# Optimization experiments

Measured on AMD Instinct MI355X. Metric: run time of the kernel, lower is better.

Reference implementation:

```python
import jax, jax.numpy as jnp
import numpy as np

TEMPERATURE = 0.1
NEG_INF = -1e30  # finite sentinel to keep logsumexp grad-safe


def setup_inputs() -> dict:
    key = jax.random.key(0)
    k_emb, k_lab = jax.random.split(key)
    B, D, C = 8192, 256, 100
    embeddings = jax.random.normal(k_emb, (B, D), dtype=jnp.float32)
    labels = jax.random.randint(k_lab, (B,), 0, C, dtype=jnp.int64)
    return {"embeddings": embeddings, "labels": labels}


def reference(embeddings, labels):
    B = embeddings.shape[0]
    # squared L2 pairwise distance: ||x_i||^2 + ||x_j||^2 - 2 x_i . x_j
    sq = jnp.sum(embeddings * embeddings, axis=1)  # [B]
    gram = jnp.einsum('id,jd->ij', embeddings, embeddings)  # [B,B]
    dist2 = jnp.maximum(sq[:, None] + sq[None, :] - 2.0 * gram, 0.0)
    sim = -dist2 / TEMPERATURE  # [B,B]

    same = labels[:, None] == labels[None, :]
    eye = jnp.eye(B, dtype=bool)
    pos_mask = same & ~eye
    neg_mask = ~same

    # per-row uniform random positive via Gumbel-argmax over pos_mask
    k_sel = jax.random.key(42)
    g = jax.random.gumbel(k_sel, (B, B), dtype=jnp.float32)
    j = jnp.argmax(jnp.where(pos_mask, g, -jnp.inf), axis=1)  # [B]

    numerator = jnp.take_along_axis(sim, j[:, None], axis=1)[:, 0]  # sim[i, j_i]
    denominator = jax.nn.logsumexp(jnp.where(neg_mask, sim, NEG_INF), axis=1)

    valid = pos_mask.any(axis=1) & neg_mask.any(axis=1)
    per_row = -(numerator - denominator)
    n_valid = jnp.sum(valid)
    loss = jnp.sum(jnp.where(valid, per_row, 0.0)) / jnp.maximum(n_valid, 1)
    return jnp.where(n_valid > 0, loss, 0.0)
```

## Files before the change

### kernel.cpp

```cpp
#include <hip/hip_runtime.h>
#include <float.h>
#include <math.h>


#define B_N 8192
#define D_K 256
#define NCLS 100
#define MAXC 512
#define NSPLIT 16
#define NPART NSPLIT
#define JR (B_N / NSPLIT)
#define BI 128
#define BJ 128
#define NJT (JR / BJ)
#define BK 64
#define NKC (D_K / BK)
#define NEG_INF -1e30f

typedef __attribute__((ext_vector_type(8))) short bf16x8;
typedef __attribute__((ext_vector_type(4))) float f32x4;
typedef unsigned short ushort_t;

__device__ __forceinline__ unsigned rotl32(unsigned x, int d){ return (x << d) | (x >> (32 - d)); }

__device__ __forceinline__ float gumbel_at(unsigned idx){
  const unsigned HALF = (unsigned)B_N * (unsigned)B_N / 2u;
  unsigned c0, c1; bool second;
  if (idx < HALF){ c0 = idx; c1 = idx + HALF; second = false; }
  else            { c0 = idx - HALF; c1 = idx; second = true; }
  const unsigned ks0 = 0u, ks1 = 42u, ks2 = 0u ^ 42u ^ 0x1BD11BDAu;
  unsigned x0 = c0 + ks0, x1 = c1 + ks1;
#define TF_RND(r) { x0 += x1; x1 = rotl32(x1, (r)); x1 ^= x0; }
  TF_RND(13) TF_RND(15) TF_RND(26) TF_RND(6)   x0 += ks1; x1 += ks2 + 1u;
  TF_RND(17) TF_RND(29) TF_RND(16) TF_RND(24)  x0 += ks2; x1 += ks0 + 2u;
  TF_RND(13) TF_RND(15) TF_RND(26) TF_RND(6)   x0 += ks0; x1 += ks1 + 3u;
  TF_RND(17) TF_RND(29) TF_RND(16) TF_RND(24)  x0 += ks1; x1 += ks2 + 4u;
  TF_RND(13) TF_RND(15) TF_RND(26) TF_RND(6)   x0 += ks2; x1 += ks0 + 5u;
#undef TF_RND
  unsigned bits = second ? x1 : x0;
  float u = __uint_as_float((bits >> 9) | 0x3f800000u) - 1.0f;
  const float TINY = 1.17549435e-38f;
  u = u * (1.0f - TINY) + TINY;
  u = fmaxf(TINY, u);
  return -logf(-logf(u));
}

__device__ __forceinline__ ushort_t f2bf(float x){
  unsigned u = __float_as_uint(x);
  return (ushort_t)((u + 0x7FFFu + ((u >> 16) & 1u)) >> 16);
}

__device__ __forceinline__ void async16(const ushort_t* g, ushort_t* lds_wave_base){
  __builtin_amdgcn_global_load_lds((const __attribute__((address_space(1))) void*)g,
                                   (__attribute__((address_space(3))) void*)lds_wave_base,
                                   16, 0, 0);
}

__global__ void prep_kernel(const float* __restrict__ E, ushort_t* __restrict__ Ebf,
                            float* __restrict__ sq, float* __restrict__ acc4){
  if (blockIdx.x == 0 && threadIdx.x < 4)
    acc4[threadIdx.x] = 0.f;
  int w = threadIdx.x >> 6, lane = threadIdx.x & 63;
  int row = blockIdx.x * 4 + w;
  const float4 v = *reinterpret_cast<const float4*>(E + (size_t)row * D_K + lane * 4);
  float s = v.x*v.x + v.y*v.y + v.z*v.z + v.w*v.w;
#pragma unroll
  for (int off = 32; off > 0; off >>= 1) s += __shfl_down(s, off);
  if (lane == 0) sq[row] = s;
  ushort4 o; o.x = f2bf(v.x); o.y = f2bf(v.y); o.z = f2bf(v.z); o.w = f2bf(v.w);
  *reinterpret_cast<ushort4*>(Ebf + (size_t)row * D_K + lane * 4) = o;
}

__global__ __launch_bounds__(256)
void classsel_kernel(const int* __restrict__ labels, int* __restrict__ jsel){
  __shared__ int s_list[MAXC];
  __shared__ int s_n;
  const int c = blockIdx.x;
  const int tid = threadIdx.x;
  if (tid == 0) s_n = 0;
  __syncthreads();
  for (int t = tid; t < B_N; t += 256){
    if (labels[t] == c){
      int p = atomicAdd(&s_n, 1);
      if (p < MAXC) s_list[p] = t;
    }
  }
  __syncthreads();
  const int n = min(s_n, MAXC);
  for (int rowIdx = tid; rowIdx < n; rowIdx += 256){
    const int row = s_list[rowIdx];
    float gb = -FLT_MAX; int jb = -1;
    for (int t = 0; t < n; t++){
      int j = s_list[t];
      if (j != row){
        float g = gumbel_at(((unsigned)row << 13) + (unsigned)j);
        if (g > gb || (g == gb && (unsigned)j < (unsigned)jb)){ gb = g; jb = j; }
      }
    }
    jsel[row] = jb;
  }
}

__global__ __launch_bounds__(256, 2)
void fused_kernel(const ushort_t* __restrict__ Ebf, const int* __restrict__ labels,
                  const float* __restrict__ sq, const int* __restrict__ jsel,
                  float* __restrict__ numer,
                  float* __restrict__ wsM, float* __restrict__ wsS)
{
  __shared__ __align__(16) ushort_t Bs[NKC][BJ * BK];
  __shared__ float s_sqj[JR];
  __shared__ int   s_lj[JR];
  __shared__ float s_sqi[BI];
  __shared__ int   s_li[BI];
  __shared__ int   s_ji[BI];

  const int bi    = blockIdx.x >> 4;
  const int split = blockIdx.x & 15;
  const int i0    = bi * BI;
  const int jbase = split * JR;
  const int tid   = threadIdx.x;
  const int lane  = tid & 63;
  const int w     = tid >> 6;
  const int quad  = lane >> 4;
  const int l15   = lane & 15;

  for (int t = tid; t < JR; t += 256){ s_sqj[t] = sq[jbase + t]; s_lj[t] = labels[jbase + t]; }
  if (tid < BI){ s_sqi[tid] = sq[i0 + tid]; s_li[tid] = labels[i0 + tid]; s_ji[tid] = jsel[i0 + tid]; }

  bf16x8 af[2][8];
#pragma unroll
  for (int mt = 0; mt < 2; mt++){
    const ushort_t* rp = Ebf + (size_t)(i0 + w * 32 + mt * 16 + l15) * D_K + quad * 8;
#pragma unroll
    for (int c = 0; c < 8; c++)
      af[mt][c] = *reinterpret_cast<const bf16x8*>(rp + c * 32);
  }

  float sm[8], ssum[8];
#pragma unroll
  for (int r = 0; r < 8; r++){ sm[r] = NEG_INF; ssum[r] = 0.f; }

  __syncthreads();

  for (int jt = 0; jt < NJT; jt++){
    const int j0 = jbase + jt * BJ;
    f32x4 acc[2][8];
#pragma unroll
    for (int mt = 0; mt < 2; mt++)
#pragma unroll
      for (int nt = 0; nt < 8; nt++) acc[mt][nt] = (f32x4)0.f;

    __syncthreads();
#pragma unroll
    for (int kc = 0; kc < NKC; kc++){
#pragma unroll
      for (int rd = 0; rd < 4; rd++){
        int slot = rd * 256 + tid;
        int r = slot >> 3, gs = slot & 7;
        int gsrc = (gs ^ (r & 7)) << 3;
        ushort_t* ldsB = &Bs[kc][(size_t)(rd * 256 + w * 64) * 8];
        async16(Ebf + (size_t)(j0 + r) * D_K + kc * BK + gsrc, ldsB);
      }
    }
    __syncthreads();

#pragma unroll
    for (int kc = 0; kc < NKC; kc++){
#pragma unroll
      for (int s = 0; s < 2; s++){
        const int g = s * 4 + quad;
        const int c = kc * 2 + s;
        bf16x8 bfr[8];
#pragma unroll
        for (int nt = 0; nt < 8; nt++){
          int r = nt * 16 + l15;
          bfr[nt] = *reinterpret_cast<const bf16x8*>(&Bs[kc][r * BK + ((g ^ (r & 7)) << 3)]);
        }
#pragma unroll
        for (int nt = 0; nt < 8; nt++){
          acc[0][nt] = __builtin_amdgcn_mfma_f32_16x16x32_bf16(af[0][c], bfr[nt], acc[0][nt], 0, 0, 0);
          acc[1][nt] = __builtin_amdgcn_mfma_f32_16x16x32_bf16(af[1][c], bfr[nt], acc[1][nt], 0, 0, 0);
        }
      }
    }

    float sqj[8]; int lj[8];
#pragma unroll
    for (int nt = 0; nt < 8; nt++){
      int ccol = jt * BJ + nt * 16 + l15;
      sqj[nt] = s_sqj[ccol]; lj[nt] = s_lj[ccol];
    }
#pragma unroll
    for (int mt = 0; mt < 2; mt++){
#pragma unroll
      for (int rr = 0; rr < 4; rr++){
        int rl = w * 32 + mt * 16 + quad * 4 + rr;
        float sqv = s_sqi[rl]; int lrow = s_li[rl]; int jsl = s_ji[rl];
        int sidx = mt * 4 + rr;
        float sv[8];
#pragma unroll
        for (int nt = 0; nt < 8; nt++){
          float a = acc[mt][nt][rr];
          float simv = -10.f * fmaxf(fmaf(-2.f, a, sqv + sqj[nt]), 0.f);
          int colg = j0 + nt * 16 + l15;
          if (colg == jsl) numer[i0 + rl] = simv;
          sv[nt] = (lj[nt] != lrow) ? simv : NEG_INF;
        }
        float m8 = fmaxf(fmaxf(fmaxf(sv[0],sv[1]),fmaxf(sv[2],sv[3])),
                         fmaxf(fmaxf(sv[4],sv[5]),fmaxf(sv[6],sv[7])));
        float s8 = __expf(sv[0]-m8)+__expf(sv[1]-m8)+__expf(sv[2]-m8)+__expf(sv[3]-m8)
                 + __expf(sv[4]-m8)+__expf(sv[5]-m8)+__expf(sv[6]-m8)+__expf(sv[7]-m8);
        float M = fmaxf(sm[sidx], m8);
        ssum[sidx] = ssum[sidx]*__expf(sm[sidx]-M) + s8*__expf(m8-M);
        sm[sidx] = M;
      }
    }
  }

#pragma unroll
  for (int sidx = 0; sidx < 8; sidx++){
    float mv = sm[sidx], sv2 = ssum[sidx];
#pragma unroll
    for (int mask = 1; mask < 16; mask <<= 1){
      float m2 = __shfl_xor(mv, mask);
      float s2 = __shfl_xor(sv2, mask);
      float M = fmaxf(mv, m2);
      sv2 = sv2 * __expf(mv - M) + s2 * __expf(m2 - M);
      mv = M;
    }
    if (l15 == 0){
      int mt = sidx >> 2, rr = sidx & 3;
      int rl = w * 32 + mt * 16 + quad * 4 + rr;
      int o = split * B_N + i0 + rl;
      wsM[o] = mv; wsS[o] = sv2;
    }
  }
}

__global__ __launch_bounds__(256)
void finale_kernel(const float* __restrict__ wsM, const float* __restrict__ wsS,
                   const float* __restrict__ numer, const int* __restrict__ jsel,
                   float* __restrict__ acc4, float* __restrict__ out)
{
  const int tid = threadIdx.x;
  const int row = blockIdx.x * 256 + tid;
  float M = -3.0e38f, S = 0.f;
#pragma unroll
  for (int p = 0; p < NPART; p++){
    float m2 = wsM[p * B_N + row], s2 = wsS[p * B_N + row];
    float Mn = fmaxf(M, m2);
    S = S * __expf(M - Mn) + s2 * __expf(m2 - Mn);
    M = Mn;
  }
  bool v = (jsel[row] >= 0) && (M > -5e29f);
  float s = v ? (M + logf(S) - numer[row]) : 0.f;
  unsigned n = v ? 1u : 0u;
#pragma unroll
  for (int off = 32; off > 0; off >>= 1){ s += __shfl_down(s, off); n += __shfl_down(n, off); }
  __shared__ float ssm[4]; __shared__ unsigned snm[4];
  if ((tid & 63) == 0){ ssm[tid >> 6] = s; snm[tid >> 6] = n; }
  __syncthreads();
  if (tid == 0){
    float bs = ssm[0] + ssm[1] + ssm[2] + ssm[3];
    unsigned bn = snm[0] + snm[1] + snm[2] + snm[3];
    atomicAdd(&acc4[0], bs);
    atomicAdd((unsigned*)&acc4[1], bn);
    __threadfence();
    unsigned old = atomicAdd((unsigned*)&acc4[2], 1u);
    if (old == 31u){
      float St = atomicAdd(&acc4[0], 0.f);
      unsigned Nt = atomicAdd((unsigned*)&acc4[1], 0u);
      out[0] = (Nt > 0u) ? (St / (float)Nt) : 0.f;
    }
  }
}

extern "C" void kernel_launch(void* const* d_in, const int* in_sizes, int n_in,
                              void* d_out, int out_size, void* d_ws, size_t ws_size,
                              hipStream_t stream)
{
  const float* E      = (const float*)d_in[0];
  const int*   labels = (const int*)d_in[1];
  float*       out    = (float*)d_out;

  ushort_t* Ebf = (ushort_t*)d_ws;
  float* wsM    = (float*)(Ebf + (size_t)B_N * D_K);
  float* wsS    = wsM + NPART * B_N;
  float* sqb    = wsS + NPART * B_N;
  float* numer  = sqb + B_N;
  int* jsel     = (int*)(numer + B_N);
  float* acc4   = (float*)(jsel + B_N);

  prep_kernel<<<B_N / 4, 256, 0, stream>>>(E, Ebf, sqb, acc4);
  classsel_kernel<<<NCLS, 256, 0, stream>>>(labels, jsel);
  fused_kernel<<<(B_N / BI) * NSPLIT, 256, 0, stream>>>(Ebf, labels, sqb, jsel, numer, wsM, wsS);
  finale_kernel<<<B_N / 256, 256, 0, stream>>>(wsM, wsS, numer, jsel, acc4, out);
}
```

Measured before the change: 164.2 us.

## Use 2x2 wave tiling, single-stage LDS buffer, fewer splits, merge prep kernels

The fused kernel now arranges its four waves in a 2x2 grid over the 128x128 tile, so each wave holds 64 rows of A fragments and reads only 64 columns of B from LDS. This halves B-fragment LDS reads per MFMA. The LDS B buffer drops from four K-chunks to one, with a sync before and after each chunk load, which adds barriers and removes the overlap between loads and MFMAs. NSPLIT falls from 16 to 8, giving fewer, longer blocks (512 instead of 1024), and each wave column writes its own partial logsumexp slot. The prep and class-selection kernels are merged into one launch to save launch overhead.

```diff
diff --git a/kernel.cpp b/kernel.cpp
--- a/kernel.cpp
+++ b/kernel.cpp
@@ -7,8 +7,8 @@
 #define D_K 256
 #define NCLS 100
 #define MAXC 512
-#define NSPLIT 16
-#define NPART NSPLIT
+#define NSPLIT 8
+#define NPART (NSPLIT * 2)
 #define JR (B_N / NSPLIT)
 #define BI 128
 #define BJ 128
@@ -16,6 +16,7 @@
 #define BK 64
 #define NKC (D_K / BK)
 #define NEG_INF -1e30f
+#define PREP_BLOCKS (B_N / 4)
 
 typedef __attribute__((ext_vector_type(8))) short bf16x8;
 typedef __attribute__((ext_vector_type(4))) float f32x4;
@@ -56,27 +57,27 @@
                                    16, 0, 0);
 }
 
-__global__ void prep_kernel(const float* __restrict__ E, ushort_t* __restrict__ Ebf,
-                            float* __restrict__ sq, float* __restrict__ acc4){
-  if (blockIdx.x == 0 && threadIdx.x < 4)
-    acc4[threadIdx.x] = 0.f;
-  int w = threadIdx.x >> 6, lane = threadIdx.x & 63;
-  int row = blockIdx.x * 4 + w;
-  const float4 v = *reinterpret_cast<const float4*>(E + (size_t)row * D_K + lane * 4);
-  float s = v.x*v.x + v.y*v.y + v.z*v.z + v.w*v.w;
-#pragma unroll
-  for (int off = 32; off > 0; off >>= 1) s += __shfl_down(s, off);
-  if (lane == 0) sq[row] = s;
-  ushort4 o; o.x = f2bf(v.x); o.y = f2bf(v.y); o.z = f2bf(v.z); o.w = f2bf(v.w);
-  *reinterpret_cast<ushort4*>(Ebf + (size_t)row * D_K + lane * 4) = o;
-}
-
 __global__ __launch_bounds__(256)
-void classsel_kernel(const int* __restrict__ labels, int* __restrict__ jsel){
+void prepsel_kernel(const float* __restrict__ E, const int* __restrict__ labels,
+                    ushort_t* __restrict__ Ebf, float* __restrict__ sq,
+                    int* __restrict__ jsel, float* __restrict__ acc4){
+  const int tid = threadIdx.x;
+  if (blockIdx.x < PREP_BLOCKS){
+    if (blockIdx.x == 0 && tid < 4) acc4[tid] = 0.f;
+    int w = tid >> 6, lane = tid & 63;
+    int row = blockIdx.x * 4 + w;
+    const float4 v = *reinterpret_cast<const float4*>(E + (size_t)row * D_K + lane * 4);
+    float s = v.x*v.x + v.y*v.y + v.z*v.z + v.w*v.w;
+#pragma unroll
+    for (int off = 32; off > 0; off >>= 1) s += __shfl_down(s, off);
+    if (lane == 0) sq[row] = s;
+    ushort4 o; o.x = f2bf(v.x); o.y = f2bf(v.y); o.z = f2bf(v.z); o.w = f2bf(v.w);
+    *reinterpret_cast<ushort4*>(Ebf + (size_t)row * D_K + lane * 4) = o;
+    return;
+  }
   __shared__ int s_list[MAXC];
   __shared__ int s_n;
-  const int c = blockIdx.x;
-  const int tid = threadIdx.x;
+  const int c = blockIdx.x - PREP_BLOCKS;
   if (tid == 0) s_n = 0;
   __syncthreads();
   for (int t = tid; t < B_N; t += 256){
@@ -107,118 +108,114 @@
                   float* __restrict__ numer,
                   float* __restrict__ wsM, float* __restrict__ wsS)
 {
-  __shared__ __align__(16) ushort_t Bs[NKC][BJ * BK];
+  __shared__ __align__(16) ushort_t Bs[BJ * BK];
   __shared__ float s_sqj[JR];
   __shared__ int   s_lj[JR];
   __shared__ float s_sqi[BI];
   __shared__ int   s_li[BI];
   __shared__ int   s_ji[BI];
 
-  const int bi    = blockIdx.x >> 4;
-  const int split = blockIdx.x & 15;
+  const int bi    = blockIdx.x >> 3;
+  const int split = blockIdx.x & 7;
   const int i0    = bi * BI;
   const int jbase = split * JR;
   const int tid   = threadIdx.x;
   const int lane  = tid & 63;
   const int w     = tid >> 6;
+  const int wy    = w >> 1;
+  const int wx    = w & 1;
   const int quad  = lane >> 4;
   const int l15   = lane & 15;
 
   for (int t = tid; t < JR; t += 256){ s_sqj[t] = sq[jbase + t]; s_lj[t] = labels[jbase + t]; }
   if (tid < BI){ s_sqi[tid] = sq[i0 + tid]; s_li[tid] = labels[i0 + tid]; s_ji[tid] = jsel[i0 + tid]; }
 
-  bf16x8 af[2][8];
-#pragma unroll
-  for (int mt = 0; mt < 2; mt++){
-    const ushort_t* rp = Ebf + (size_t)(i0 + w * 32 + mt * 16 + l15) * D_K + quad * 8;
+  bf16x8 af[4][8];
+#pragma unroll
+  for (int mt = 0; mt < 4; mt++){
+    const ushort_t* rp = Ebf + (size_t)(i0 + wy * 64 + mt * 16 + l15) * D_K + quad * 8;
 #pragma unroll
     for (int c = 0; c < 8; c++)
       af[mt][c] = *reinterpret_cast<const bf16x8*>(rp + c * 32);
   }
 
-  float sm[8], ssum[8];
-#pragma unroll
-  for (int r = 0; r < 8; r++){ sm[r] = NEG_INF; ssum[r] = 0.f; }
+  float sm[16], ssum[16];
+#pragma unroll
+  for (int r = 0; r < 16; r++){ sm[r] = NEG_INF; ssum[r] = 0.f; }
 
   __syncthreads();
 
   for (int jt = 0; jt < NJT; jt++){
     const int j0 = jbase + jt * BJ;
-    f32x4 acc[2][8];
-#pragma unroll
-    for (int mt = 0; mt < 2; mt++)
-#pragma unroll
-      for (int nt = 0; nt < 8; nt++) acc[mt][nt] = (f32x4)0.f;
-
-    __syncthreads();
-#pragma unroll
+    f32x4 acc[4][4];
+#pragma unroll
+    for (int mt = 0; mt < 4; mt++)
+#pragma unroll
+      for (int nt = 0; nt < 4; nt++) acc[mt][nt] = (f32x4)0.f;
+
     for (int kc = 0; kc < NKC; kc++){
+      const int koff = kc * BK;
+      __syncthreads();
 #pragma unroll
       for (int rd = 0; rd < 4; rd++){
         int slot = rd * 256 + tid;
         int r = slot >> 3, gs = slot & 7;
         int gsrc = (gs ^ (r & 7)) << 3;
-        ushort_t* ldsB = &Bs[kc][(size_t)(rd * 256 + w * 64) * 8];
-        async16(Ebf + (size_t)(j0 + r) * D_K + kc * BK + gsrc, ldsB);
-      }
-    }
-    __syncthreads();
-
-#pragma unroll
-    for (int kc = 0; kc < NKC; kc++){
+        ushort_t* ldsB = Bs + (size_t)(rd * 256 + w * 64) * 8;
+        async16(Ebf + (size_t)(j0 + r) * D_K + koff + gsrc, ldsB);
+      }
+      __syncthreads();
 #pragma unroll
       for (int s = 0; s < 2; s++){
         const int g = s * 4 + quad;
         const int c = kc * 2 + s;
-        bf16x8 bfr[8];
-#pragma unroll
-        for (int nt = 0; nt < 8; nt++){
-          int r = nt * 16 + l15;
-          bfr[nt] = *reinterpret_cast<const bf16x8*>(&Bs[kc][r * BK + ((g ^ (r & 7)) << 3)]);
+        bf16x8 bfr[4];
+#pragma unroll
+        for (int nt = 0; nt < 4; nt++){
+          int r = wx * 64 + nt * 16 + l15;
+          bfr[nt] = *reinterpret_cast<const bf16x8*>(&Bs[r * BK + ((g ^ (r & 7)) << 3)]);
         }
 #pragma unroll
-        for (int nt = 0; nt < 8; nt++){
-          acc[0][nt] = __builtin_amdgcn_mfma_f32_16x16x32_bf16(af[0][c], bfr[nt], acc[0][nt], 0, 0, 0);
-          acc[1][nt] = __builtin_amdgcn_mfma_f32_16x16x32_bf16(af[1][c], bfr[nt], acc[1][nt], 0, 0, 0);
-        }
-      }
-    }
-
-    float sqj[8]; int lj[8];
-#pragma unroll
-    for (int nt = 0; nt < 8; nt++){
-      int ccol = jt * BJ + nt * 16 + l15;
+        for (int mt = 0; mt < 4; mt++)
+#pragma unroll
+          for (int nt = 0; nt < 4; nt++)
+            acc[mt][nt] = __builtin_amdgcn_mfma_f32_16x16x32_bf16(af[mt][c], bfr[nt], acc[mt][nt], 0, 0, 0);
+      }
+    }
+
+    float sqj[4]; int lj[4];
+#pragma unroll
+    for (int nt = 0; nt < 4; nt++){
+      int ccol = jt * BJ + wx * 64 + nt * 16 + l15;
       sqj[nt] = s_sqj[ccol]; lj[nt] = s_lj[ccol];
     }
 #pragma unroll
-    for (int mt = 0; mt < 2; mt++){
+    for (int mt = 0; mt < 4; mt++){
 #pragma unroll
       for (int rr = 0; rr < 4; rr++){
-        int rl = w * 32 + mt * 16 + quad * 4 + rr;
+        int rl = wy * 64 + mt * 16 + quad * 4 + rr;
         float sqv = s_sqi[rl]; int lrow = s_li[rl]; int jsl = s_ji[rl];
         int sidx = mt * 4 + rr;
-        float sv[8];
-#pragma unroll
-        for (int nt = 0; nt < 8; nt++){
+        float sv[4];
+#pragma unroll
+        for (int nt = 0; nt < 4; nt++){
           float a = acc[mt][nt][rr];
           float simv = -10.f * fmaxf(fmaf(-2.f, a, sqv + sqj[nt]), 0.f);
-          int colg = j0 + nt * 16 + l15;
+          int colg = j0 + wx * 64 + nt * 16 + l15;
           if (colg == jsl) numer[i0 + rl] = simv;
           sv[nt] = (lj[nt] != lrow) ? simv : NEG_INF;
         }
-        float m8 = fmaxf(fmaxf(fmaxf(sv[0],sv[1]),fmaxf(sv[2],sv[3])),
-                         fmaxf(fmaxf(sv[4],sv[5]),fmaxf(sv[6],sv[7])));
-        float s8 = __expf(sv[0]-m8)+__expf(sv[1]-m8)+__expf(sv[2]-m8)+__expf(sv[3]-m8)
-                 + __expf(sv[4]-m8)+__expf(sv[5]-m8)+__expf(sv[6]-m8)+__expf(sv[7]-m8);
-        float M = fmaxf(sm[sidx], m8);
-        ssum[sidx] = ssum[sidx]*__expf(sm[sidx]-M) + s8*__expf(m8-M);
+        float m4 = fmaxf(fmaxf(sv[0], sv[1]), fmaxf(sv[2], sv[3]));
+        float s4 = __expf(sv[0]-m4) + __expf(sv[1]-m4) + __expf(sv[2]-m4) + __expf(sv[3]-m4);
+        float M = fmaxf(sm[sidx], m4);
+        ssum[sidx] = ssum[sidx]*__expf(sm[sidx]-M) + s4*__expf(m4-M);
         sm[sidx] = M;
       }
     }
   }
 
 #pragma unroll
-  for (int sidx = 0; sidx < 8; sidx++){
+  for (int sidx = 0; sidx < 16; sidx++){
     float mv = sm[sidx], sv2 = ssum[sidx];
 #pragma unroll
     for (int mask = 1; mask < 16; mask <<= 1){
@@ -230,8 +227,8 @@
     }
     if (l15 == 0){
       int mt = sidx >> 2, rr = sidx & 3;
-      int rl = w * 32 + mt * 16 + quad * 4 + rr;
-      int o = split * B_N + i0 + rl;
+      int rl = wy * 64 + mt * 16 + quad * 4 + rr;
+      int o = (split * 2 + wx) * B_N + i0 + rl;
       wsM[o] = mv; wsS[o] = sv2;
     }
   }
@@ -291,8 +288,7 @@
   int* jsel     = (int*)(numer + B_N);
   float* acc4   = (float*)(jsel + B_N);
 
-  prep_kernel<<<B_N / 4, 256, 0, stream>>>(E, Ebf, sqb, acc4);
-  classsel_kernel<<<NCLS, 256, 0, stream>>>(labels, jsel);
+  prepsel_kernel<<<PREP_BLOCKS + NCLS, 256, 0, stream>>>(E, labels, Ebf, sqb, jsel, acc4);
   fused_kernel<<<(B_N / BI) * NSPLIT, 256, 0, stream>>>(Ebf, labels, sqb, jsel, numer, wsM, wsS);
   finale_kernel<<<B_N / 256, 256, 0, stream>>>(wsM, wsS, numer, jsel, acc4, out);
 }
```

Result: slower. 196.0 us (+19.4%).

## Double-buffer B tiles, merge prep/select kernels, fold finale into fused kernel

Applied to the files above, without the earlier changes.

Replaces the load-all-then-compute B staging with a two-slot ring buffer, so the async load of the next k-chunk overlaps MFMA work on the current one. Halves the j-split count, which gives fewer, longer blocks and fewer partial rows to merge. Merges the prep and class-select kernels into one launch and moves the final reduction into the last-finishing fused block via an atomic ticket, removing two launches. The risks are a serial single-block finale over all 8192 rows and a smaller grid (512 blocks) that may underfill the GPU.

```diff
diff --git a/kernel.cpp b/kernel.cpp
--- a/kernel.cpp
+++ b/kernel.cpp
@@ -7,7 +7,7 @@
 #define D_K 256
 #define NCLS 100
 #define MAXC 512
-#define NSPLIT 16
+#define NSPLIT 8
 #define NPART NSPLIT
 #define JR (B_N / NSPLIT)
 #define BI 128
@@ -15,7 +15,10 @@
 #define NJT (JR / BJ)
 #define BK 64
 #define NKC (D_K / BK)
+#define NSTEP (NJT * NKC)
 #define NEG_INF -1e30f
+#define PREP_BLOCKS (B_N / 4)
+#define GRID_FUSED ((B_N / BI) * NSPLIT)
 
 typedef __attribute__((ext_vector_type(8))) short bf16x8;
 typedef __attribute__((ext_vector_type(4))) float f32x4;
@@ -56,27 +59,39 @@
                                    16, 0, 0);
 }
 
-__global__ void prep_kernel(const float* __restrict__ E, ushort_t* __restrict__ Ebf,
-                            float* __restrict__ sq, float* __restrict__ acc4){
-  if (blockIdx.x == 0 && threadIdx.x < 4)
-    acc4[threadIdx.x] = 0.f;
-  int w = threadIdx.x >> 6, lane = threadIdx.x & 63;
-  int row = blockIdx.x * 4 + w;
-  const float4 v = *reinterpret_cast<const float4*>(E + (size_t)row * D_K + lane * 4);
-  float s = v.x*v.x + v.y*v.y + v.z*v.z + v.w*v.w;
-#pragma unroll
-  for (int off = 32; off > 0; off >>= 1) s += __shfl_down(s, off);
-  if (lane == 0) sq[row] = s;
-  ushort4 o; o.x = f2bf(v.x); o.y = f2bf(v.y); o.z = f2bf(v.z); o.w = f2bf(v.w);
-  *reinterpret_cast<ushort4*>(Ebf + (size_t)row * D_K + lane * 4) = o;
+__device__ __forceinline__ void stageB(const ushort_t* __restrict__ Ebf, int j0, int koff,
+                                       ushort_t* buf, int tid, int w){
+#pragma unroll
+  for (int rd = 0; rd < 4; rd++){
+    int slot = rd * 256 + tid;
+    int r = slot >> 3, gs = slot & 7;
+    int gsrc = (gs ^ (r & 7)) << 3;
+    ushort_t* ldsB = buf + (size_t)(rd * 256 + w * 64) * 8;
+    async16(Ebf + (size_t)(j0 + r) * D_K + koff + gsrc, ldsB);
+  }
 }
 
 __global__ __launch_bounds__(256)
-void classsel_kernel(const int* __restrict__ labels, int* __restrict__ jsel){
+void prepsel_kernel(const float* __restrict__ E, const int* __restrict__ labels,
+                    ushort_t* __restrict__ Ebf, float* __restrict__ sq,
+                    int* __restrict__ jsel, float* __restrict__ acc4){
+  const int tid = threadIdx.x;
+  if (blockIdx.x < PREP_BLOCKS){
+    if (blockIdx.x == 0 && tid < 4) acc4[tid] = 0.f;
+    int w = tid >> 6, lane = tid & 63;
+    int row = blockIdx.x * 4 + w;
+    const float4 v = *reinterpret_cast<const float4*>(E + (size_t)row * D_K + lane * 4);
+    float s = v.x*v.x + v.y*v.y + v.z*v.z + v.w*v.w;
+#pragma unroll
+    for (int off = 32; off > 0; off >>= 1) s += __shfl_down(s, off);
+    if (lane == 0) sq[row] = s;
+    ushort4 o; o.x = f2bf(v.x); o.y = f2bf(v.y); o.z = f2bf(v.z); o.w = f2bf(v.w);
+    *reinterpret_cast<ushort4*>(Ebf + (size_t)row * D_K + lane * 4) = o;
+    return;
+  }
   __shared__ int s_list[MAXC];
   __shared__ int s_n;
-  const int c = blockIdx.x;
-  const int tid = threadIdx.x;
+  const int c = blockIdx.x - PREP_BLOCKS;
   if (tid == 0) s_n = 0;
   __syncthreads();
   for (int t = tid; t < B_N; t += 256){
@@ -105,17 +120,20 @@
 void fused_kernel(const ushort_t* __restrict__ Ebf, const int* __restrict__ labels,
                   const float* __restrict__ sq, const int* __restrict__ jsel,
                   float* __restrict__ numer,
-                  float* __restrict__ wsM, float* __restrict__ wsS)
+                  float* __restrict__ wsM, float* __restrict__ wsS,
+                  float* __restrict__ acc4, float* __restrict__ out)
 {
-  __shared__ __align__(16) ushort_t Bs[NKC][BJ * BK];
+  __shared__ __align__(16) ushort_t Bs[2][BJ * BK];
   __shared__ float s_sqj[JR];
   __shared__ int   s_lj[JR];
   __shared__ float s_sqi[BI];
   __shared__ int   s_li[BI];
   __shared__ int   s_ji[BI];
-
-  const int bi    = blockIdx.x >> 4;
-  const int split = blockIdx.x & 15;
+  __shared__ unsigned s_tk;
+  __shared__ float ssm[4]; __shared__ unsigned snm[4];
+
+  const int bi    = blockIdx.x >> 3;
+  const int split = blockIdx.x & 7;
   const int i0    = bi * BI;
   const int jbase = split * JR;
   const int tid   = threadIdx.x;
@@ -140,7 +158,7 @@
 #pragma unroll
   for (int r = 0; r < 8; r++){ sm[r] = NEG_INF; ssum[r] = 0.f; }
 
-  __syncthreads();
+  stageB(Ebf, jbase, 0, Bs[0], tid, w);
 
   for (int jt = 0; jt < NJT; jt++){
     const int j0 = jbase + jt * BJ;
@@ -150,36 +168,30 @@
 #pragma unroll
       for (int nt = 0; nt < 8; nt++) acc[mt][nt] = (f32x4)0.f;
 
-    __syncthreads();
 #pragma unroll
     for (int kc = 0; kc < NKC; kc++){
-#pragma unroll
-      for (int rd = 0; rd < 4; rd++){
-        int slot = rd * 256 + tid;
-        int r = slot >> 3, gs = slot & 7;
-        int gsrc = (gs ^ (r & 7)) << 3;
-        ushort_t* ldsB = &Bs[kc][(size_t)(rd * 256 + w * 64) * 8];
-        async16(Ebf + (size_t)(j0 + r) * D_K + kc * BK + gsrc, ldsB);
-      }
-    }
-    __syncthreads();
-
-#pragma unroll
-    for (int kc = 0; kc < NKC; kc++){
+      const int cur = kc & 1;
+      __syncthreads();
+      {
+        int step = jt * NKC + kc + 1;
+        if (step < NSTEP){
+          int njt = step >> 2, nkc = step & 3;
+          stageB(Ebf, jbase + njt * BJ, nkc * BK, Bs[cur ^ 1], tid, w);
+        }
+      }
 #pragma unroll
       for (int s = 0; s < 2; s++){
         const int g = s * 4 + quad;
-        const int c = kc * 2 + s;
         bf16x8 bfr[8];
 #pragma unroll
         for (int nt = 0; nt < 8; nt++){
           int r = nt * 16 + l15;
-          bfr[nt] = *reinterpret_cast<const bf16x8*>(&Bs[kc][r * BK + ((g ^ (r & 7)) << 3)]);
+          bfr[nt] = *reinterpret_cast<const bf16x8*>(&Bs[cur][r * BK + ((g ^ (r & 7)) << 3)]);
         }
 #pragma unroll
         for (int nt = 0; nt < 8; nt++){
-          acc[0][nt] = __builtin_amdgcn_mfma_f32_16x16x32_bf16(af[0][c], bfr[nt], acc[0][nt], 0, 0, 0);
-          acc[1][nt] = __builtin_amdgcn_mfma_f32_16x16x32_bf16(af[1][c], bfr[nt], acc[1][nt], 0, 0, 0);
+          acc[0][nt] = __builtin_amdgcn_mfma_f32_16x16x32_bf16(af[0][kc * 2 + s], bfr[nt], acc[0][nt], 0, 0, 0);
+          acc[1][nt] = __builtin_amdgcn_mfma_f32_16x16x32_bf16(af[1][kc * 2 + s], bfr[nt], acc[1][nt], 0, 0, 0);
         }
       }
     }
@@ -235,41 +247,32 @@
       wsM[o] = mv; wsS[o] = sv2;
     }
   }
-}
-
-__global__ __launch_bounds__(256)
-void finale_kernel(const float* __restrict__ wsM, const float* __restrict__ wsS,
-                   const float* __restrict__ numer, const int* __restrict__ jsel,
-                   float* __restrict__ acc4, float* __restrict__ out)
-{
-  const int tid = threadIdx.x;
-  const int row = blockIdx.x * 256 + tid;
-  float M = -3.0e38f, S = 0.f;
-#pragma unroll
-  for (int p = 0; p < NPART; p++){
-    float m2 = wsM[p * B_N + row], s2 = wsS[p * B_N + row];
-    float Mn = fmaxf(M, m2);
-    S = S * __expf(M - Mn) + s2 * __expf(m2 - Mn);
-    M = Mn;
-  }
-  bool v = (jsel[row] >= 0) && (M > -5e29f);
-  float s = v ? (M + logf(S) - numer[row]) : 0.f;
-  unsigned n = v ? 1u : 0u;
-#pragma unroll
-  for (int off = 32; off > 0; off >>= 1){ s += __shfl_down(s, off); n += __shfl_down(n, off); }
-  __shared__ float ssm[4]; __shared__ unsigned snm[4];
-  if ((tid & 63) == 0){ ssm[tid >> 6] = s; snm[tid >> 6] = n; }
+
+  __threadfence();
+  if (tid == 0) s_tk = atomicAdd((unsigned*)acc4 + 3, 1u);
   __syncthreads();
-  if (tid == 0){
-    float bs = ssm[0] + ssm[1] + ssm[2] + ssm[3];
-    unsigned bn = snm[0] + snm[1] + snm[2] + snm[3];
-    atomicAdd(&acc4[0], bs);
-    atomicAdd((unsigned*)&acc4[1], bn);
+  if (s_tk == (unsigned)(GRID_FUSED - 1)){
     __threadfence();
-    unsigned old = atomicAdd((unsigned*)&acc4[2], 1u);
-    if (old == 31u){
-      float St = atomicAdd(&acc4[0], 0.f);
-      unsigned Nt = atomicAdd((unsigned*)&acc4[1], 0u);
+    float s = 0.f; unsigned n = 0u;
+    for (int row = tid; row < B_N; row += 256){
+      float M = -3.0e38f, S = 0.f;
+#pragma unroll
+      for (int p = 0; p < NPART; p++){
+        float m2 = wsM[p * B_N + row], s2 = wsS[p * B_N + row];
+        float Mn = fmaxf(M, m2);
+        S = S * __expf(M - Mn) + s2 * __expf(m2 - Mn);
+        M = Mn;
+      }
+      bool v = (jsel[row] >= 0) && (M > -5e29f);
+      if (v){ s += M + logf(S) - numer[row]; n += 1u; }
+    }
+#pragma unroll
+    for (int off = 32; off > 0; off >>= 1){ s += __shfl_down(s, off); n += __shfl_down(n, off); }
+    if ((tid & 63) == 0){ ssm[tid >> 6] = s; snm[tid >> 6] = n; }
+    __syncthreads();
+    if (tid == 0){
+      float St = ssm[0] + ssm[1] + ssm[2] + ssm[3];
+      unsigned Nt = snm[0] + snm[1] + snm[2] + snm[3];
       out[0] = (Nt > 0u) ? (St / (float)Nt) : 0.f;
     }
   }
@@ -291,8 +294,6 @@
   int* jsel     = (int*)(numer + B_N);
   float* acc4   = (float*)(jsel + B_N);
 
-  prep_kernel<<<B_N / 4, 256, 0, stream>>>(E, Ebf, sqb, acc4);
-  classsel_kernel<<<NCLS, 256, 0, stream>>>(labels, jsel);
-  fused_kernel<<<(B_N / BI) * NSPLIT, 256, 0, stream>>>(Ebf, labels, sqb, jsel, numer, wsM, wsS);
-  finale_kernel<<<B_N / 256, 256, 0, stream>>>(wsM, wsS, numer, jsel, acc4, out);
-}
+  prepsel_kernel<<<PREP_BLOCKS + NCLS, 256, 0, stream>>>(E, labels, Ebf, sqb, jsel, acc4);
+  fused_kernel<<<GRID_FUSED, 256, 0, stream>>>(Ebf, labels, sqb, jsel, numer, wsM, wsS, acc4, out);
+}
```

Result: slower. 236.3 us (+43.9%).

## Merge prep and class-select kernels; shrink B tile LDS to one K-chunk

Applied to the files above, without the earlier changes.

Folds the bf16 conversion/norm kernel and the per-class Gumbel selection kernel into one launch, so the two independent jobs share a grid and one kernel launch is dropped. In the fused GEMM kernel, the B tile LDS buffer shrinks from all four K-chunks to a single chunk, reloaded per chunk with barriers around it. This cuts LDS use, which may allow more resident blocks, but adds synchronisation and serialises load and compute within each j-tile.

```diff
diff --git a/kernel.cpp b/kernel.cpp
--- a/kernel.cpp
+++ b/kernel.cpp
@@ -16,6 +16,7 @@
 #define BK 64
 #define NKC (D_K / BK)
 #define NEG_INF -1e30f
+#define PREP_BLOCKS (B_N / 4)
 
 typedef __attribute__((ext_vector_type(8))) short bf16x8;
 typedef __attribute__((ext_vector_type(4))) float f32x4;
@@ -56,27 +57,27 @@
                                    16, 0, 0);
 }
 
-__global__ void prep_kernel(const float* __restrict__ E, ushort_t* __restrict__ Ebf,
-                            float* __restrict__ sq, float* __restrict__ acc4){
-  if (blockIdx.x == 0 && threadIdx.x < 4)
-    acc4[threadIdx.x] = 0.f;
-  int w = threadIdx.x >> 6, lane = threadIdx.x & 63;
-  int row = blockIdx.x * 4 + w;
-  const float4 v = *reinterpret_cast<const float4*>(E + (size_t)row * D_K + lane * 4);
-  float s = v.x*v.x + v.y*v.y + v.z*v.z + v.w*v.w;
-#pragma unroll
-  for (int off = 32; off > 0; off >>= 1) s += __shfl_down(s, off);
-  if (lane == 0) sq[row] = s;
-  ushort4 o; o.x = f2bf(v.x); o.y = f2bf(v.y); o.z = f2bf(v.z); o.w = f2bf(v.w);
-  *reinterpret_cast<ushort4*>(Ebf + (size_t)row * D_K + lane * 4) = o;
-}
-
 __global__ __launch_bounds__(256)
-void classsel_kernel(const int* __restrict__ labels, int* __restrict__ jsel){
+void prepsel_kernel(const float* __restrict__ E, const int* __restrict__ labels,
+                    ushort_t* __restrict__ Ebf, float* __restrict__ sq,
+                    int* __restrict__ jsel, float* __restrict__ acc4){
+  const int tid = threadIdx.x;
+  if (blockIdx.x < PREP_BLOCKS){
+    if (blockIdx.x == 0 && tid < 4) acc4[tid] = 0.f;
+    int w = tid >> 6, lane = tid & 63;
+    int row = blockIdx.x * 4 + w;
+    const float4 v = *reinterpret_cast<const float4*>(E + (size_t)row * D_K + lane * 4);
+    float s = v.x*v.x + v.y*v.y + v.z*v.z + v.w*v.w;
+#pragma unroll
+    for (int off = 32; off > 0; off >>= 1) s += __shfl_down(s, off);
+    if (lane == 0) sq[row] = s;
+    ushort4 o; o.x = f2bf(v.x); o.y = f2bf(v.y); o.z = f2bf(v.z); o.w = f2bf(v.w);
+    *reinterpret_cast<ushort4*>(Ebf + (size_t)row * D_K + lane * 4) = o;
+    return;
+  }
   __shared__ int s_list[MAXC];
   __shared__ int s_n;
-  const int c = blockIdx.x;
-  const int tid = threadIdx.x;
+  const int c = blockIdx.x - PREP_BLOCKS;
   if (tid == 0) s_n = 0;
   __syncthreads();
   for (int t = tid; t < B_N; t += 256){
@@ -107,7 +108,7 @@
                   float* __restrict__ numer,
                   float* __restrict__ wsM, float* __restrict__ wsS)
 {
-  __shared__ __align__(16) ushort_t Bs[NKC][BJ * BK];
+  __shared__ __align__(16) ushort_t Bs[BJ * BK];
   __shared__ float s_sqj[JR];
   __shared__ int   s_lj[JR];
   __shared__ float s_sqi[BI];
@@ -150,36 +151,32 @@
 #pragma unroll
       for (int nt = 0; nt < 8; nt++) acc[mt][nt] = (f32x4)0.f;
 
-    __syncthreads();
 #pragma unroll
     for (int kc = 0; kc < NKC; kc++){
+      const int koff = kc * BK;
+      __syncthreads();
 #pragma unroll
       for (int rd = 0; rd < 4; rd++){
         int slot = rd * 256 + tid;
         int r = slot >> 3, gs = slot & 7;
         int gsrc = (gs ^ (r & 7)) << 3;
-        ushort_t* ldsB = &Bs[kc][(size_t)(rd * 256 + w * 64) * 8];
-        async16(Ebf + (size_t)(j0 + r) * D_K + kc * BK + gsrc, ldsB);
-      }
-    }
-    __syncthreads();
-
-#pragma unroll
-    for (int kc = 0; kc < NKC; kc++){
+        ushort_t* ldsB = Bs + (size_t)(rd * 256 + w * 64) * 8;
+        async16(Ebf + (size_t)(j0 + r) * D_K + koff + gsrc, ldsB);
+      }
+      __syncthreads();
 #pragma unroll
       for (int s = 0; s < 2; s++){
         const int g = s * 4 + quad;
-        const int c = kc * 2 + s;
         bf16x8 bfr[8];
 #pragma unroll
         for (int nt = 0; nt < 8; nt++){
           int r = nt * 16 + l15;
-          bfr[nt] = *reinterpret_cast<const bf16x8*>(&Bs[kc][r * BK + ((g ^ (r & 7)) << 3)]);
+          bfr[nt] = *reinterpret_cast<const bf16x8*>(&Bs[r * BK + ((g ^ (r & 7)) << 3)]);
         }
 #pragma unroll
         for (int nt = 0; nt < 8; nt++){
-          acc[0][nt] = __builtin_amdgcn_mfma_f32_16x16x32_bf16(af[0][c], bfr[nt], acc[0][nt], 0, 0, 0);
-          acc[1][nt] = __builtin_amdgcn_mfma_f32_16x16x32_bf16(af[1][c], bfr[nt], acc[1][nt], 0, 0, 0);
+          acc[0][nt] = __builtin_amdgcn_mfma_f32_16x16x32_bf16(af[0][kc * 2 + s], bfr[nt], acc[0][nt], 0, 0, 0);
+          acc[1][nt] = __builtin_amdgcn_mfma_f32_16x16x32_bf16(af[1][kc * 2 + s], bfr[nt], acc[1][nt], 0, 0, 0);
         }
       }
     }
@@ -291,8 +288,7 @@
   int* jsel     = (int*)(numer + B_N);
   float* acc4   = (float*)(jsel + B_N);
 
-  prep_kernel<<<B_N / 4, 256, 0, stream>>>(E, Ebf, sqb, acc4);
-  classsel_kernel<<<NCLS, 256, 0, stream>>>(labels, jsel);
+  prepsel_kernel<<<PREP_BLOCKS + NCLS, 256, 0, stream>>>(E, labels, Ebf, sqb, jsel, acc4);
   fused_kernel<<<(B_N / BI) * NSPLIT, 256, 0, stream>>>(Ebf, labels, sqb, jsel, numer, wsM, wsS);
   finale_kernel<<<B_N / 256, 256, 0, stream>>>(wsM, wsS, numer, jsel, acc4, out);
 }
```

Result: slower. 170.7 us (+3.9%).
